# Kernel tuning notes

Hardware: AMD Instinct MI355X
Metric: run time of the kernel (lower is better)

Reference implementation:

```python
import jax, jax.numpy as jnp
import numpy as np

B, T, D = 8, 1024, 128
TEMP = 0.1
WEIGHT = 1.0


def _neg_scaled_l2(x, y):
    # x: [P, T, D], y: [P, S, D] -> -||x-y||^2 / D / TEMP  (l2 similarity, normalize_dimension=True)
    x2 = jnp.sum(x * x, axis=-1)[..., :, None]            # [P, T, 1]
    y2 = jnp.sum(y * y, axis=-1)[..., None, :]            # [P, 1, S]
    xy = jnp.einsum('ptd,psd->pts', x, y)                 # [P, T, S]
    d2 = jnp.maximum(x2 + y2 - 2.0 * xy, 0.0)             # cdist(...)**2 is non-negative
    return -d2 / D / TEMP


def setup_inputs() -> dict:
    key = jax.random.key(0)
    k1, k2, k3 = jax.random.split(key, 3)
    embs = jax.random.normal(k1, (B, T, D), dtype=jnp.float32)
    frame_idxs = jnp.sort(jax.random.randint(k2, (B, T), 0, 4096, dtype=jnp.int32), axis=-1)
    video_len = jax.random.randint(k3, (B,), T, 4096, dtype=jnp.int32)
    return {"embs": embs, "frame_idxs": frame_idxs, "video_len": video_len}


def reference(embs, frame_idxs, video_len):
    # All ordered pairs (i, j) with i != j, built at trace time.
    pairs = np.array([(i, j) for i in range(B) for j in range(B) if i != j])
    ii, jj = pairs[:, 0], pairs[:, 1]                     # [P]

    e1 = embs[ii]                                         # [P, T, D]
    e2 = embs[jj]                                         # [P, T, D]

    # Cycle: soft nearest neighbors of e1 in e2, then align back to e1.
    sim12 = _neg_scaled_l2(e1, e2)                        # [P, T, T]
    beta12 = jax.nn.softmax(sim12, axis=-1)
    nn_embs = jnp.einsum('pts,psd->ptd', beta12, e2)      # [P, T, D]
    logits = _neg_scaled_l2(nn_embs, e1)                  # [P, T, T]

    beta = jax.nn.softmax(logits, axis=-1)                # [P, T, T]
    steps = frame_idxs.astype(jnp.float32) / video_len.astype(jnp.float32)[:, None]  # [B, T]
    sp = steps[ii]                                        # [P, T] (steps of sequence i)
    time_true = sp                                        # one_hot(labels) picks the diagonal
    time_pred = jnp.einsum('pts,ps->pt', beta, sp)        # [P, T]
    loss = jnp.mean((time_pred - time_true) ** 2)
    return WEIGHT * loss
```

## Files before the change

### kernel.cpp

```cpp
#include <hip/hip_runtime.h>
#include <hip/hip_bf16.h>


#define T_ 1024
#define D_ 128
#define NPAIR 56
#define NSCALE 0.11271055006945026f
#define SQDS 0.474785316f

typedef float f32x16 __attribute__((ext_vector_type(16)));
typedef unsigned short u16x8 __attribute__((ext_vector_type(8)));

#define B8F 131072
#define B8T 163840

__device__ __forceinline__ unsigned short f2bf(float f) {
  unsigned u = __float_as_uint(f);
  u += 0x7fff + ((u >> 16) & 1);
  return (unsigned short)(u >> 16);
}
__device__ __forceinline__ float bf2f(unsigned short v) {
  return __uint_as_float(((unsigned)v) << 16);
}
__device__ __forceinline__ float clamp8(float x) {
  return fminf(fmaxf(x, -440.f), 440.f);
}
__device__ __forceinline__ unsigned pk4(float a, float b, float c, float d) {
  int w = __builtin_amdgcn_cvt_pk_fp8_f32(a, b, 0, false);
  w = __builtin_amdgcn_cvt_pk_fp8_f32(c, d, w, true);
  return (unsigned)w;
}
__device__ __forceinline__ float waveSum(float v) {
#pragma unroll
  for (int k = 32; k >= 1; k >>= 1) v += __shfl_xor(v, k, 64);
  return v;
}
__device__ __forceinline__ void stage1k(const unsigned char* g, unsigned char* lds, int lane) {
  __builtin_amdgcn_global_load_lds(
      (const __attribute__((address_space(1))) unsigned int*)(g + lane * 16),
      (__attribute__((address_space(3))) unsigned int*)lds, 16, 0, 0);
}

__device__ __forceinline__ void c2b8(const unsigned* m, int lh, long long* b0, long long* b1) {
  unsigned send0 = lh ? m[0] : m[1];
  unsigned send1 = lh ? m[2] : m[3];
  unsigned r0 = (unsigned)__shfl_xor((int)send0, 32, 64);
  unsigned r1 = (unsigned)__shfl_xor((int)send1, 32, 64);
  union { unsigned u[2]; long long ll; } x0, x1;
  x0.u[0] = lh ? r0 : m[0];  x0.u[1] = lh ? m[1] : r0;
  x1.u[0] = lh ? r1 : m[2];  x1.u[1] = lh ? m[3] : r1;
  *b0 = x0.ll; *b1 = x1.ll;
}

#define MFMA8(A, B, C) __builtin_amdgcn_mfma_f32_32x32x16_fp8_fp8((A), (B), (C), 0, 0, 0)
#define LD8(P, Q) (*(const long long*)((P) + (Q) * 512))
#define EXPC(x) fminf(__builtin_amdgcn_exp2f(x), 448.f)

__global__ __launch_bounds__(256) void convert_kernel(
    const float* __restrict__ embs, const int* __restrict__ fi,
    const int* __restrict__ vl, unsigned char* __restrict__ e8F,
    unsigned char* __restrict__ e8T, float* __restrict__ steps,
    float* __restrict__ acc, unsigned* __restrict__ cnt) {
  __shared__ unsigned short tileS[32 * 136];
  __shared__ float psum[32][8];
  __shared__ float g_sh[32], sp_sh[32];
  const int b = blockIdx.x >> 5;
  const int t0 = (blockIdx.x & 31) * 32;
  const int tid = threadIdx.x;
  const int row = tid >> 3, seg = tid & 7;

  if (blockIdx.x == 0 && tid == 0) { acc[0] = 0.f; cnt[0] = 0u; }

  const float* src = embs + (size_t)(b * T_ + t0 + row) * D_ + seg * 16;
  float4 g4[4];
#pragma unroll
  for (int k = 0; k < 4; k++) g4[k] = ((const float4*)src)[k];
  float s = 0.f;
  float fv[16];
#pragma unroll
  for (int k = 0; k < 4; k++) {
    s += g4[k].x * g4[k].x + g4[k].y * g4[k].y + g4[k].z * g4[k].z + g4[k].w * g4[k].w;
    fv[4 * k + 0] = g4[k].x * SQDS; fv[4 * k + 1] = g4[k].y * SQDS;
    fv[4 * k + 2] = g4[k].z * SQDS; fv[4 * k + 3] = g4[k].w * SQDS;
  }
  psum[row][seg] = s;

  {
    unsigned char* dstA = e8F + (size_t)b * B8F + (size_t)((t0 >> 5) * 8 + seg) * 512;
    uint2 lo, hi;
    lo.x = pk4(fv[0], fv[1], fv[2], fv[3]);   lo.y = pk4(fv[4], fv[5], fv[6], fv[7]);
    hi.x = pk4(fv[8], fv[9], fv[10], fv[11]); hi.y = pk4(fv[12], fv[13], fv[14], fv[15]);
    *(uint2*)(dstA + row * 8) = lo;
    *(uint2*)(dstA + (size_t)(32 + row) * 8) = hi;
  }
#pragma unroll
  for (int k = 0; k < 16; k++) tileS[row * 136 + seg * 16 + k] = f2bf(fv[k]);
  __syncthreads();

  if (tid < 32) {
    float t = 0.f;
#pragma unroll
    for (int k = 0; k < 8; k++) t += psum[tid][k];
    int gr = b * T_ + t0 + tid;
    float sp = (float)fi[gr] / (float)vl[b];
    steps[gr] = sp;
    sp_sh[tid] = sp;
    g_sh[tid] = __builtin_amdgcn_exp2f(14.0f - t * NSCALE);
  }
  __syncthreads();

  {
    const int c8 = tid >> 5;
    const int n2 = c8 & 3, scp = c8 >> 2;
    const int dd = n2 * 32 + (tid & 31);
#pragma unroll
    for (int half = 0; half < 2; half++) {
      const int lane = half * 32 + (tid & 31);
      const int sl = scp * 16 + half * 8;
      float vv[8];
#pragma unroll
      for (int jj = 0; jj < 8; jj++)
        vv[jj] = clamp8(bf2f(tileS[(sl + jj) * 136 + dd]) * g_sh[sl + jj]);
      uint2 wv;
      wv.x = pk4(vv[0], vv[1], vv[2], vv[3]);
      wv.y = pk4(vv[4], vv[5], vv[6], vv[7]);
      int c = n2 * 64 + (t0 >> 4) + scp;
      *(uint2*)(e8T + (size_t)b * B8T + (size_t)c * 512 + lane * 8) = wv;
    }
  }
  if (tid < 128) {
    const int sc2 = tid >> 6, lane = tid & 63;
    const int m = lane & 31, kh = lane >> 5;
    uint2 wv; wv.x = 0u; wv.y = 0u;
    if (m < 2) {
      float vv[8];
#pragma unroll
      for (int e = 0; e < 8; e++) {
        int sl = sc2 * 16 + kh * 8 + e;
        float gg = g_sh[sl];
        vv[e] = clamp8(m ? gg * sp_sh[sl] : gg);
      }
      wv.x = pk4(vv[0], vv[1], vv[2], vv[3]);
      wv.y = pk4(vv[4], vv[5], vv[6], vv[7]);
    }
    int c = 256 + (t0 >> 4) + sc2;
    *(uint2*)(e8T + (size_t)b * B8T + (size_t)c * 512 + lane * 8) = wv;
  }
}

__global__ __launch_bounds__(256, 2) void tcc_main(
    const unsigned char* __restrict__ e8F, const unsigned char* __restrict__ e8T,
    const float* __restrict__ steps, float* __restrict__ loss_acc,
    unsigned* __restrict__ cnt, float* __restrict__ out) {
  __shared__ unsigned char smem[40960];
  __shared__ float blred[4];
  unsigned char* kt = smem;
  unsigned char* vt = smem + 16384;
  unsigned char* gt = smem + 36864;

  const int bx = blockIdx.x;
  const int pair = bx >> 3;
  const int tile = bx & 7;
  const int i = pair / 7;
  const int r = pair % 7;
  const int j = r + (r >= i ? 1 : 0);
  const int tid = threadIdx.x;
  const int w = tid >> 6;
  const int l = tid & 63;
  const int l31 = l & 31;
  const int lh = l >> 5;
  const int tb = tile * 128 + w * 32;

  const unsigned char* eFi = e8F + (size_t)i * B8F;
  const unsigned char* eFj = e8F + (size_t)j * B8F;
  const unsigned char* eTj = e8T + (size_t)j * B8T;
  const unsigned char* eTi = e8T + (size_t)i * B8T;

  long long qf8[8];
  {
    const unsigned char* qb = eFi + (size_t)((tb >> 5) * 8) * 512 + l * 8;
#pragma unroll
    for (int kc = 0; kc < 8; kc++) qf8[kc] = LD8(qb, kc);
  }

  const f32x16 Z = {0.f, 0.f, 0.f, 0.f, 0.f, 0.f, 0.f, 0.f,
                    0.f, 0.f, 0.f, 0.f, 0.f, 0.f, 0.f, 0.f};
  const f32x16 CM6 = {-6.f, -6.f, -6.f, -6.f, -6.f, -6.f, -6.f, -6.f,
                      -6.f, -6.f, -6.f, -6.f, -6.f, -6.f, -6.f, -6.f};
  f32x16 o[5];
#pragma unroll
  for (int n2 = 0; n2 < 5; n2++) o[n2] = Z;

  stage1k(eFj + (size_t)(2 * w) * 1024, kt + (2 * w) * 1024, l);
  stage1k(eFj + (size_t)(2 * w + 1) * 1024, kt + (2 * w + 1) * 1024, l);
#pragma unroll
  for (int u = 0; u < 3; u++) {
    int vu = w + 4 * u;
    if (vu < 10) {
      int n2v = vu >> 1, sh = vu & 1;
      stage1k(eTj + (size_t)(n2v * 32 + sh) * 1024, vt + vu * 1024, l);
    }
  }
  __syncthreads();

  for (int st = 0; st < 16; st++) {
    const int cur = st & 1, nxt = cur ^ 1;
    if (st < 15) {
      const int s1 = st + 1;
      stage1k(eFj + (size_t)(8 * s1 + 2 * w) * 1024, kt + nxt * 8192 + (2 * w) * 1024, l);
      stage1k(eFj + (size_t)(8 * s1 + 2 * w + 1) * 1024, kt + nxt * 8192 + (2 * w + 1) * 1024, l);
#pragma unroll
      for (int u = 0; u < 3; u++) {
        int vu = w + 4 * u;
        if (vu < 10) {
          int n2v = vu >> 1, sh = vu & 1;
          stage1k(eTj + (size_t)(n2v * 32 + s1 * 2 + sh) * 1024, vt + nxt * 10240 + vu * 1024, l);
        }
      }
    }
    __builtin_amdgcn_sched_barrier(0);

    const unsigned char* kb = kt + cur * 8192 + l * 8;
    const unsigned char* vb = vt + cur * 10240 + l * 8;

    f32x16 ca0 = MFMA8(LD8(kb, 0), qf8[0], CM6);
    f32x16 ca1 = MFMA8(LD8(kb, 8), qf8[0], CM6);
#pragma unroll
    for (int dc = 1; dc < 8; dc++) {
      ca0 = MFMA8(LD8(kb, dc), qf8[dc], ca0);
      ca1 = MFMA8(LD8(kb, 8 + dc), qf8[dc], ca1);
    }
    unsigned m0[4], m1[4];
#pragma unroll
    for (int k2 = 0; k2 < 4; k2++) {
      m0[k2] = pk4(EXPC(ca0[4 * k2]), EXPC(ca0[4 * k2 + 1]),
                   EXPC(ca0[4 * k2 + 2]), EXPC(ca0[4 * k2 + 3]));
      m1[k2] = pk4(EXPC(ca1[4 * k2]), EXPC(ca1[4 * k2 + 1]),
                   EXPC(ca1[4 * k2 + 2]), EXPC(ca1[4 * k2 + 3]));
    }
    long long pB[4];
    c2b8(m0, lh, &pB[0], &pB[1]);
    c2b8(m1, lh, &pB[2], &pB[3]);
#pragma unroll
    for (int n2 = 0; n2 < 5; n2++)
#pragma unroll
      for (int sc = 0; sc < 4; sc++)
        o[n2] = MFMA8(LD8(vb, n2 * 4 + sc), pB[sc], o[n2]);
    __syncthreads();
  }

  stage1k(eFi + (size_t)(2 * w) * 1024, kt + (2 * w) * 1024, l);
  stage1k(eFi + (size_t)(2 * w + 1) * 1024, kt + (2 * w + 1) * 1024, l);
  if (w < 2) stage1k(eTi + (size_t)(128 + w) * 1024, gt + w * 1024, l);

  float Lme = o[4][0];
  float Lo = __shfl_xor(Lme, 32, 64);
  float inv = 1.0f / (lh ? Lo : Lme);
  long long qf2[8];
#pragma unroll
  for (int n2 = 0; n2 < 4; n2++) {
    unsigned mm[4];
#pragma unroll
    for (int k2 = 0; k2 < 4; k2++)
      mm[k2] = pk4(o[n2][4 * k2] * inv, o[n2][4 * k2 + 1] * inv,
                   o[n2][4 * k2 + 2] * inv, o[n2][4 * k2 + 3] * inv);
    c2b8(mm, lh, &qf2[2 * n2], &qf2[2 * n2 + 1]);
  }
  f32x16 acc6 = Z;
  __syncthreads();

  for (int st = 0; st < 16; st++) {
    const int cur = st & 1, nxt = cur ^ 1;
    if (st < 15) {
      const int s1 = st + 1;
      stage1k(eFi + (size_t)(8 * s1 + 2 * w) * 1024, kt + nxt * 8192 + (2 * w) * 1024, l);
      stage1k(eFi + (size_t)(8 * s1 + 2 * w + 1) * 1024, kt + nxt * 8192 + (2 * w + 1) * 1024, l);
      if (w < 2) stage1k(eTi + (size_t)(128 + s1 * 2 + w) * 1024, gt + nxt * 2048 + w * 1024, l);
    }
    __builtin_amdgcn_sched_barrier(0);

    const unsigned char* kb = kt + cur * 8192 + l * 8;
    const unsigned char* gb = gt + cur * 2048 + l * 8;

    f32x16 ca0 = MFMA8(LD8(kb, 0), qf2[0], CM6);
    f32x16 ca1 = MFMA8(LD8(kb, 8), qf2[0], CM6);
#pragma unroll
    for (int dc = 1; dc < 8; dc++) {
      ca0 = MFMA8(LD8(kb, dc), qf2[dc], ca0);
      ca1 = MFMA8(LD8(kb, 8 + dc), qf2[dc], ca1);
    }
    unsigned m0[4], m1[4];
#pragma unroll
    for (int k2 = 0; k2 < 4; k2++) {
      m0[k2] = pk4(EXPC(ca0[4 * k2]), EXPC(ca0[4 * k2 + 1]),
                   EXPC(ca0[4 * k2 + 2]), EXPC(ca0[4 * k2 + 3]));
      m1[k2] = pk4(EXPC(ca1[4 * k2]), EXPC(ca1[4 * k2 + 1]),
                   EXPC(ca1[4 * k2 + 2]), EXPC(ca1[4 * k2 + 3]));
    }
    long long pB[4];
    c2b8(m0, lh, &pB[0], &pB[1]);
    c2b8(m1, lh, &pB[2], &pB[3]);
#pragma unroll
    for (int sc = 0; sc < 4; sc++)
      acc6 = MFMA8(LD8(gb, sc), pB[sc], acc6);
    __syncthreads();
  }

  float local = 0.f;
  if (lh == 0) {
    float pred = acc6[1] / acc6[0];
    float tt = steps[i * T_ + tb + l31];
    float dd = pred - tt;
    local = dd * dd;
  }
  local = waveSum(local);
  if (l == 0) blred[w] = local;
  __syncthreads();
  if (tid == 0) {
    atomicAdd(loss_acc, blred[0] + blred[1] + blred[2] + blred[3]);
    __threadfence();
    unsigned old = atomicAdd(cnt, 1u);
    if (old == (unsigned)(gridDim.x - 1)) {
      float v = atomicAdd(loss_acc, 0.0f);
      out[0] = v * (1.0f / (float)(NPAIR * T_));
    }
  }
}

extern "C" void kernel_launch(void* const* d_in, const int* in_sizes, int n_in,
                              void* d_out, int out_size, void* d_ws, size_t ws_size,
                              hipStream_t stream) {
  const float* embs = (const float*)d_in[0];
  const int* frame_idxs = (const int*)d_in[1];
  const int* video_len = (const int*)d_in[2];
  float* out = (float*)d_out;

  char* ws = (char*)d_ws;
  float* acc = (float*)ws;
  unsigned* cnt = (unsigned*)(ws + 512);
  float* steps = (float*)(ws + 4096);
  unsigned char* e8F = (unsigned char*)(ws + 65536);
  unsigned char* e8T = e8F + (size_t)8 * B8F;

  convert_kernel<<<dim3(256), dim3(256), 0, stream>>>(embs, frame_idxs, video_len,
                                                      e8F, e8T, steps, acc, cnt);
  tcc_main<<<dim3(NPAIR * 8), dim3(256), 0, stream>>>(e8F, e8T, steps, acc, cnt, out);
}
```

Before: 114.5 us.

## Split key dimension across warp pairs and double grid with cross-warp reduction

Each block now covers 64 query rows instead of 128. The four warps split into two row groups, each handling half of every 32-key stage (split-K). Partial flash-attention accumulators are combined through shared memory, and the normalized second-stage queries are shared the same way. The grid doubles to 896 blocks and launch bounds ask for 3 blocks per CU to improve occupancy and CU fill. In exchange, global staging traffic per row doubles and extra LDS reductions and barriers are added.

```diff
diff --git a/kernel.cpp b/kernel.cpp
--- a/kernel.cpp
+++ b/kernel.cpp
@@ -148,28 +148,30 @@
   }
 }
 
-__global__ __launch_bounds__(256, 2) void tcc_main(
+__global__ __launch_bounds__(256, 3) void tcc_main(
     const unsigned char* __restrict__ e8F, const unsigned char* __restrict__ e8T,
     const float* __restrict__ steps, float* __restrict__ loss_acc,
     unsigned* __restrict__ cnt, float* __restrict__ out) {
-  __shared__ unsigned char smem[40960];
+  __shared__ unsigned char smem[49152];
   __shared__ float blred[4];
   unsigned char* kt = smem;
   unsigned char* vt = smem + 16384;
   unsigned char* gt = smem + 36864;
 
   const int bx = blockIdx.x;
-  const int pair = bx >> 3;
-  const int tile = bx & 7;
+  const int pair = bx >> 4;
+  const int tile = bx & 15;
   const int i = pair / 7;
   const int r = pair % 7;
   const int j = r + (r >= i ? 1 : 0);
   const int tid = threadIdx.x;
   const int w = tid >> 6;
+  const int rg = w & 1;
+  const int sh = w >> 1;
   const int l = tid & 63;
   const int l31 = l & 31;
   const int lh = l >> 5;
-  const int tb = tile * 128 + w * 32;
+  const int tb = tile * 64 + rg * 32;
 
   const unsigned char* eFi = e8F + (size_t)i * B8F;
   const unsigned char* eFj = e8F + (size_t)j * B8F;
@@ -197,8 +199,8 @@
   for (int u = 0; u < 3; u++) {
     int vu = w + 4 * u;
     if (vu < 10) {
-      int n2v = vu >> 1, sh = vu & 1;
-      stage1k(eTj + (size_t)(n2v * 32 + sh) * 1024, vt + vu * 1024, l);
+      int n2v = vu >> 1, uh = vu & 1;
+      stage1k(eTj + (size_t)(n2v * 32 + uh) * 1024, vt + vu * 1024, l);
     }
   }
   __syncthreads();
@@ -213,59 +215,76 @@
       for (int u = 0; u < 3; u++) {
         int vu = w + 4 * u;
         if (vu < 10) {
-          int n2v = vu >> 1, sh = vu & 1;
-          stage1k(eTj + (size_t)(n2v * 32 + s1 * 2 + sh) * 1024, vt + nxt * 10240 + vu * 1024, l);
+          int n2v = vu >> 1, uh = vu & 1;
+          stage1k(eTj + (size_t)(n2v * 32 + s1 * 2 + uh) * 1024, vt + nxt * 10240 + vu * 1024, l);
         }
       }
     }
     __builtin_amdgcn_sched_barrier(0);
 
-    const unsigned char* kb = kt + cur * 8192 + l * 8;
-    const unsigned char* vb = vt + cur * 10240 + l * 8;
-
-    f32x16 ca0 = MFMA8(LD8(kb, 0), qf8[0], CM6);
-    f32x16 ca1 = MFMA8(LD8(kb, 8), qf8[0], CM6);
-#pragma unroll
-    for (int dc = 1; dc < 8; dc++) {
-      ca0 = MFMA8(LD8(kb, dc), qf8[dc], ca0);
-      ca1 = MFMA8(LD8(kb, 8 + dc), qf8[dc], ca1);
-    }
-    unsigned m0[4], m1[4];
-#pragma unroll
-    for (int k2 = 0; k2 < 4; k2++) {
-      m0[k2] = pk4(EXPC(ca0[4 * k2]), EXPC(ca0[4 * k2 + 1]),
-                   EXPC(ca0[4 * k2 + 2]), EXPC(ca0[4 * k2 + 3]));
-      m1[k2] = pk4(EXPC(ca1[4 * k2]), EXPC(ca1[4 * k2 + 1]),
-                   EXPC(ca1[4 * k2 + 2]), EXPC(ca1[4 * k2 + 3]));
-    }
-    long long pB[4];
+    const unsigned char* kb = kt + cur * 8192 + sh * 4096 + l * 8;
+    const unsigned char* vb = vt + cur * 10240 + sh * 1024 + l * 8;
+
+    f32x16 ca = MFMA8(LD8(kb, 0), qf8[0], CM6);
+#pragma unroll
+    for (int dc = 1; dc < 8; dc++) ca = MFMA8(LD8(kb, dc), qf8[dc], ca);
+    unsigned m0[4];
+#pragma unroll
+    for (int k2 = 0; k2 < 4; k2++)
+      m0[k2] = pk4(EXPC(ca[4 * k2]), EXPC(ca[4 * k2 + 1]),
+                   EXPC(ca[4 * k2 + 2]), EXPC(ca[4 * k2 + 3]));
+    long long pB[2];
     c2b8(m0, lh, &pB[0], &pB[1]);
-    c2b8(m1, lh, &pB[2], &pB[3]);
 #pragma unroll
     for (int n2 = 0; n2 < 5; n2++)
 #pragma unroll
-      for (int sc = 0; sc < 4; sc++)
+      for (int sc = 0; sc < 2; sc++)
         o[n2] = MFMA8(LD8(vb, n2 * 4 + sc), pB[sc], o[n2]);
     __syncthreads();
+  }
+
+  float* xb = (float*)smem;
+  if (sh == 1) {
+#pragma unroll
+    for (int n2 = 0; n2 < 5; n2++)
+#pragma unroll
+      for (int rr = 0; rr < 16; rr++)
+        xb[(n2 * 16 + rr) * 128 + rg * 64 + l] = o[n2][rr];
+  }
+  __syncthreads();
+  long long qf2[8];
+  if (sh == 0) {
+#pragma unroll
+    for (int n2 = 0; n2 < 5; n2++)
+#pragma unroll
+      for (int rr = 0; rr < 16; rr++)
+        o[n2][rr] += xb[(n2 * 16 + rr) * 128 + rg * 64 + l];
+    float Lme = o[4][0];
+    float Lo = __shfl_xor(Lme, 32, 64);
+    float inv = 1.0f / (lh ? Lo : Lme);
+#pragma unroll
+    for (int n2 = 0; n2 < 4; n2++) {
+      unsigned mm[4];
+#pragma unroll
+      for (int k2 = 0; k2 < 4; k2++)
+        mm[k2] = pk4(o[n2][4 * k2] * inv, o[n2][4 * k2 + 1] * inv,
+                     o[n2][4 * k2 + 2] * inv, o[n2][4 * k2 + 3] * inv);
+      c2b8(mm, lh, &qf2[2 * n2], &qf2[2 * n2 + 1]);
+    }
+    long long* qb2 = (long long*)(smem + 40960);
+#pragma unroll
+    for (int kc = 0; kc < 8; kc++) qb2[kc * 128 + rg * 64 + l] = qf2[kc];
+  }
+  __syncthreads();
+  if (sh == 1) {
+    const long long* qb2 = (const long long*)(smem + 40960);
+#pragma unroll
+    for (int kc = 0; kc < 8; kc++) qf2[kc] = qb2[kc * 128 + rg * 64 + l];
   }
 
   stage1k(eFi + (size_t)(2 * w) * 1024, kt + (2 * w) * 1024, l);
   stage1k(eFi + (size_t)(2 * w + 1) * 1024, kt + (2 * w + 1) * 1024, l);
   if (w < 2) stage1k(eTi + (size_t)(128 + w) * 1024, gt + w * 1024, l);
-
-  float Lme = o[4][0];
-  float Lo = __shfl_xor(Lme, 32, 64);
-  float inv = 1.0f / (lh ? Lo : Lme);
-  long long qf2[8];
-#pragma unroll
-  for (int n2 = 0; n2 < 4; n2++) {
-    unsigned mm[4];
-#pragma unroll
-    for (int k2 = 0; k2 < 4; k2++)
-      mm[k2] = pk4(o[n2][4 * k2] * inv, o[n2][4 * k2 + 1] * inv,
-                   o[n2][4 * k2 + 2] * inv, o[n2][4 * k2 + 3] * inv);
-    c2b8(mm, lh, &qf2[2 * n2], &qf2[2 * n2 + 1]);
-  }
   f32x16 acc6 = Z;
   __syncthreads();
 
@@ -279,36 +298,36 @@
     }
     __builtin_amdgcn_sched_barrier(0);
 
-    const unsigned char* kb = kt + cur * 8192 + l * 8;
-    const unsigned char* gb = gt + cur * 2048 + l * 8;
-
-    f32x16 ca0 = MFMA8(LD8(kb, 0), qf2[0], CM6);
-    f32x16 ca1 = MFMA8(LD8(kb, 8), qf2[0], CM6);
-#pragma unroll
-    for (int dc = 1; dc < 8; dc++) {
-      ca0 = MFMA8(LD8(kb, dc), qf2[dc], ca0);
-      ca1 = MFMA8(LD8(kb, 8 + dc), qf2[dc], ca1);
-    }
-    unsigned m0[4], m1[4];
-#pragma unroll
-    for (int k2 = 0; k2 < 4; k2++) {
-      m0[k2] = pk4(EXPC(ca0[4 * k2]), EXPC(ca0[4 * k2 + 1]),
-                   EXPC(ca0[4 * k2 + 2]), EXPC(ca0[4 * k2 + 3]));
-      m1[k2] = pk4(EXPC(ca1[4 * k2]), EXPC(ca1[4 * k2 + 1]),
-                   EXPC(ca1[4 * k2 + 2]), EXPC(ca1[4 * k2 + 3]));
-    }
-    long long pB[4];
+    const unsigned char* kb = kt + cur * 8192 + sh * 4096 + l * 8;
+    const unsigned char* gb = gt + cur * 2048 + sh * 1024 + l * 8;
+
+    f32x16 ca = MFMA8(LD8(kb, 0), qf2[0], CM6);
+#pragma unroll
+    for (int dc = 1; dc < 8; dc++) ca = MFMA8(LD8(kb, dc), qf2[dc], ca);
+    unsigned m0[4];
+#pragma unroll
+    for (int k2 = 0; k2 < 4; k2++)
+      m0[k2] = pk4(EXPC(ca[4 * k2]), EXPC(ca[4 * k2 + 1]),
+                   EXPC(ca[4 * k2 + 2]), EXPC(ca[4 * k2 + 3]));
+    long long pB[2];
     c2b8(m0, lh, &pB[0], &pB[1]);
-    c2b8(m1, lh, &pB[2], &pB[3]);
-#pragma unroll
-    for (int sc = 0; sc < 4; sc++)
+#pragma unroll
+    for (int sc = 0; sc < 2; sc++)
       acc6 = MFMA8(LD8(gb, sc), pB[sc], acc6);
     __syncthreads();
   }
 
+  float* ab = (float*)(smem + 40960);
+  if (sh == 1) {
+    ab[(rg * 64 + l) * 2] = acc6[0];
+    ab[(rg * 64 + l) * 2 + 1] = acc6[1];
+  }
+  __syncthreads();
   float local = 0.f;
-  if (lh == 0) {
-    float pred = acc6[1] / acc6[0];
+  if (sh == 0 && lh == 0) {
+    float L2v = acc6[0] + ab[(rg * 64 + l) * 2];
+    float tpv = acc6[1] + ab[(rg * 64 + l) * 2 + 1];
+    float pred = tpv / L2v;
     float tt = steps[i * T_ + tb + l31];
     float dd = pred - tt;
     local = dd * dd;
@@ -344,5 +363,5 @@
 
   convert_kernel<<<dim3(256), dim3(256), 0, stream>>>(embs, frame_idxs, video_len,
                                                       e8F, e8T, steps, acc, cnt);
-  tcc_main<<<dim3(NPAIR * 8), dim3(256), 0, stream>>>(e8F, e8T, steps, acc, cnt, out);
-}
+  tcc_main<<<dim3(NPAIR * 16), dim3(256), 0, stream>>>(e8F, e8T, steps, acc, cnt, out);
+}
```

After: 130.9 us. 1.14x slower.

## Triple-buffer LDS staging with partial vmcnt waits and raw barriers

Applied to the files above, without the earlier changes.

Replaces the double-buffered LDS pipeline in both attention phases with a three-stage ring buffer that prefetches two steps ahead. A partial s_waitcnt vmcnt, tuned per wave to its number of outstanding async loads, lets each wave wait only for the oldest stage before a raw s_barrier, instead of a full __syncthreads drain. The goal is to hide global-to-LDS latency better. In exchange LDS use grows to about 54 KB per block, which may limit occupancy at two blocks per CU, and correctness now rests on hand-counted vmcnt values.

```diff
diff --git a/kernel.cpp b/kernel.cpp
--- a/kernel.cpp
+++ b/kernel.cpp
@@ -55,6 +55,8 @@
 #define MFMA8(A, B, C) __builtin_amdgcn_mfma_f32_32x32x16_fp8_fp8((A), (B), (C), 0, 0, 0)
 #define LD8(P, Q) (*(const long long*)((P) + (Q) * 512))
 #define EXPC(x) fminf(__builtin_amdgcn_exp2f(x), 448.f)
+#define WAITV(N) asm volatile("s_waitcnt vmcnt(" #N ")" ::: "memory")
+#define BAR() do { asm volatile("" ::: "memory"); __builtin_amdgcn_s_barrier(); asm volatile("" ::: "memory"); } while (0)
 
 __global__ __launch_bounds__(256) void convert_kernel(
     const float* __restrict__ embs, const int* __restrict__ fi,
@@ -152,11 +154,11 @@
     const unsigned char* __restrict__ e8F, const unsigned char* __restrict__ e8T,
     const float* __restrict__ steps, float* __restrict__ loss_acc,
     unsigned* __restrict__ cnt, float* __restrict__ out) {
-  __shared__ unsigned char smem[40960];
+  __shared__ unsigned char smem[55296];
   __shared__ float blred[4];
   unsigned char* kt = smem;
-  unsigned char* vt = smem + 16384;
-  unsigned char* gt = smem + 36864;
+  unsigned char* vt = smem + 24576;
+  unsigned char* gt = smem + 24576;
 
   const int bx = blockIdx.x;
   const int pair = bx >> 3;
@@ -191,67 +193,78 @@
 #pragma unroll
   for (int n2 = 0; n2 < 5; n2++) o[n2] = Z;
 
-  stage1k(eFj + (size_t)(2 * w) * 1024, kt + (2 * w) * 1024, l);
-  stage1k(eFj + (size_t)(2 * w + 1) * 1024, kt + (2 * w + 1) * 1024, l);
-#pragma unroll
-  for (int u = 0; u < 3; u++) {
-    int vu = w + 4 * u;
-    if (vu < 10) {
-      int n2v = vu >> 1, sh = vu & 1;
-      stage1k(eTj + (size_t)(n2v * 32 + sh) * 1024, vt + vu * 1024, l);
-    }
-  }
-  __syncthreads();
-
-  for (int st = 0; st < 16; st++) {
-    const int cur = st & 1, nxt = cur ^ 1;
-    if (st < 15) {
-      const int s1 = st + 1;
-      stage1k(eFj + (size_t)(8 * s1 + 2 * w) * 1024, kt + nxt * 8192 + (2 * w) * 1024, l);
-      stage1k(eFj + (size_t)(8 * s1 + 2 * w + 1) * 1024, kt + nxt * 8192 + (2 * w + 1) * 1024, l);
-#pragma unroll
-      for (int u = 0; u < 3; u++) {
-        int vu = w + 4 * u;
-        if (vu < 10) {
-          int n2v = vu >> 1, sh = vu & 1;
-          stage1k(eTj + (size_t)(n2v * 32 + s1 * 2 + sh) * 1024, vt + nxt * 10240 + vu * 1024, l);
-        }
-      }
-    }
-    __builtin_amdgcn_sched_barrier(0);
-
-    const unsigned char* kb = kt + cur * 8192 + l * 8;
-    const unsigned char* vb = vt + cur * 10240 + l * 8;
-
-    f32x16 ca0 = MFMA8(LD8(kb, 0), qf8[0], CM6);
-    f32x16 ca1 = MFMA8(LD8(kb, 8), qf8[0], CM6);
-#pragma unroll
-    for (int dc = 1; dc < 8; dc++) {
-      ca0 = MFMA8(LD8(kb, dc), qf8[dc], ca0);
-      ca1 = MFMA8(LD8(kb, 8 + dc), qf8[dc], ca1);
-    }
-    unsigned m0[4], m1[4];
-#pragma unroll
-    for (int k2 = 0; k2 < 4; k2++) {
-      m0[k2] = pk4(EXPC(ca0[4 * k2]), EXPC(ca0[4 * k2 + 1]),
-                   EXPC(ca0[4 * k2 + 2]), EXPC(ca0[4 * k2 + 3]));
-      m1[k2] = pk4(EXPC(ca1[4 * k2]), EXPC(ca1[4 * k2 + 1]),
-                   EXPC(ca1[4 * k2 + 2]), EXPC(ca1[4 * k2 + 3]));
-    }
-    long long pB[4];
-    c2b8(m0, lh, &pB[0], &pB[1]);
-    c2b8(m1, lh, &pB[2], &pB[3]);
-#pragma unroll
-    for (int n2 = 0; n2 < 5; n2++)
-#pragma unroll
-      for (int sc = 0; sc < 4; sc++)
-        o[n2] = MFMA8(LD8(vb, n2 * 4 + sc), pB[sc], o[n2]);
-    __syncthreads();
-  }
-
-  stage1k(eFi + (size_t)(2 * w) * 1024, kt + (2 * w) * 1024, l);
-  stage1k(eFi + (size_t)(2 * w + 1) * 1024, kt + (2 * w + 1) * 1024, l);
-  if (w < 2) stage1k(eTi + (size_t)(128 + w) * 1024, gt + w * 1024, l);
+  auto stageP1 = [&](int t, int b) {
+    stage1k(eFj + (size_t)(8 * t + 2 * w) * 1024, kt + b * 8192 + (2 * w) * 1024, l);
+    stage1k(eFj + (size_t)(8 * t + 2 * w + 1) * 1024, kt + b * 8192 + (2 * w + 1) * 1024, l);
+#pragma unroll
+    for (int u = 0; u < 3; u++) {
+      int vu = w + 4 * u;
+      if (vu < 10) {
+        int n2v = vu >> 1, uh = vu & 1;
+        stage1k(eTj + (size_t)(n2v * 32 + t * 2 + uh) * 1024, vt + b * 10240 + vu * 1024, l);
+      }
+    }
+  };
+  auto stageP2 = [&](int t, int b) {
+    stage1k(eFi + (size_t)(8 * t + 2 * w) * 1024, kt + b * 8192 + (2 * w) * 1024, l);
+    stage1k(eFi + (size_t)(8 * t + 2 * w + 1) * 1024, kt + b * 8192 + (2 * w + 1) * 1024, l);
+    if (w < 2) stage1k(eTi + (size_t)(128 + t * 2 + w) * 1024, gt + b * 2048 + w * 1024, l);
+  };
+
+  stageP1(0, 0);
+  stageP1(1, 1);
+  if (w < 2) WAITV(5); else WAITV(4);
+  BAR();
+
+  {
+    int cur = 0, pre = 2;
+    for (int st = 0; st < 16; st++) {
+      if (st <= 13) stageP1(st + 2, pre);
+      __builtin_amdgcn_sched_barrier(0);
+
+      const unsigned char* kb = kt + cur * 8192 + l * 8;
+      const unsigned char* vb = vt + cur * 10240 + l * 8;
+
+      f32x16 ca0 = MFMA8(LD8(kb, 0), qf8[0], CM6);
+      f32x16 ca1 = MFMA8(LD8(kb, 8), qf8[0], CM6);
+#pragma unroll
+      for (int dc = 1; dc < 8; dc++) {
+        ca0 = MFMA8(LD8(kb, dc), qf8[dc], ca0);
+        ca1 = MFMA8(LD8(kb, 8 + dc), qf8[dc], ca1);
+      }
+      unsigned m0[4], m1[4];
+#pragma unroll
+      for (int k2 = 0; k2 < 4; k2++) {
+        m0[k2] = pk4(EXPC(ca0[4 * k2]), EXPC(ca0[4 * k2 + 1]),
+                     EXPC(ca0[4 * k2 + 2]), EXPC(ca0[4 * k2 + 3]));
+        m1[k2] = pk4(EXPC(ca1[4 * k2]), EXPC(ca1[4 * k2 + 1]),
+                     EXPC(ca1[4 * k2 + 2]), EXPC(ca1[4 * k2 + 3]));
+      }
+      long long pB[4];
+      c2b8(m0, lh, &pB[0], &pB[1]);
+      c2b8(m1, lh, &pB[2], &pB[3]);
+#pragma unroll
+      for (int n2 = 0; n2 < 5; n2++)
+#pragma unroll
+        for (int sc = 0; sc < 4; sc++)
+          o[n2] = MFMA8(LD8(vb, n2 * 4 + sc), pB[sc], o[n2]);
+
+      if (st <= 13) {
+        if (w < 2) WAITV(5); else WAITV(4);
+        BAR();
+      } else if (st == 14) {
+        WAITV(0);
+        BAR();
+      } else {
+        BAR();
+      }
+      cur = (cur == 2) ? 0 : cur + 1;
+      pre = (pre == 2) ? 0 : pre + 1;
+    }
+  }
+
+  stageP2(0, 0);
+  stageP2(1, 1);
 
   float Lme = o[4][0];
   float Lo = __shfl_xor(Lme, 32, 64);
@@ -267,43 +280,50 @@
     c2b8(mm, lh, &qf2[2 * n2], &qf2[2 * n2 + 1]);
   }
   f32x16 acc6 = Z;
-  __syncthreads();
-
-  for (int st = 0; st < 16; st++) {
-    const int cur = st & 1, nxt = cur ^ 1;
-    if (st < 15) {
-      const int s1 = st + 1;
-      stage1k(eFi + (size_t)(8 * s1 + 2 * w) * 1024, kt + nxt * 8192 + (2 * w) * 1024, l);
-      stage1k(eFi + (size_t)(8 * s1 + 2 * w + 1) * 1024, kt + nxt * 8192 + (2 * w + 1) * 1024, l);
-      if (w < 2) stage1k(eTi + (size_t)(128 + s1 * 2 + w) * 1024, gt + nxt * 2048 + w * 1024, l);
-    }
-    __builtin_amdgcn_sched_barrier(0);
-
-    const unsigned char* kb = kt + cur * 8192 + l * 8;
-    const unsigned char* gb = gt + cur * 2048 + l * 8;
-
-    f32x16 ca0 = MFMA8(LD8(kb, 0), qf2[0], CM6);
-    f32x16 ca1 = MFMA8(LD8(kb, 8), qf2[0], CM6);
-#pragma unroll
-    for (int dc = 1; dc < 8; dc++) {
-      ca0 = MFMA8(LD8(kb, dc), qf2[dc], ca0);
-      ca1 = MFMA8(LD8(kb, 8 + dc), qf2[dc], ca1);
-    }
-    unsigned m0[4], m1[4];
-#pragma unroll
-    for (int k2 = 0; k2 < 4; k2++) {
-      m0[k2] = pk4(EXPC(ca0[4 * k2]), EXPC(ca0[4 * k2 + 1]),
-                   EXPC(ca0[4 * k2 + 2]), EXPC(ca0[4 * k2 + 3]));
-      m1[k2] = pk4(EXPC(ca1[4 * k2]), EXPC(ca1[4 * k2 + 1]),
-                   EXPC(ca1[4 * k2 + 2]), EXPC(ca1[4 * k2 + 3]));
-    }
-    long long pB[4];
-    c2b8(m0, lh, &pB[0], &pB[1]);
-    c2b8(m1, lh, &pB[2], &pB[3]);
-#pragma unroll
-    for (int sc = 0; sc < 4; sc++)
-      acc6 = MFMA8(LD8(gb, sc), pB[sc], acc6);
-    __syncthreads();
+  if (w < 2) WAITV(3); else WAITV(2);
+  BAR();
+
+  {
+    int cur = 0, pre = 2;
+    for (int st = 0; st < 16; st++) {
+      if (st <= 13) stageP2(st + 2, pre);
+      __builtin_amdgcn_sched_barrier(0);
+
+      const unsigned char* kb = kt + cur * 8192 + l * 8;
+      const unsigned char* gb = gt + cur * 2048 + l * 8;
+
+      f32x16 ca0 = MFMA8(LD8(kb, 0), qf2[0], CM6);
+      f32x16 ca1 = MFMA8(LD8(kb, 8), qf2[0], CM6);
+#pragma unroll
+      for (int dc = 1; dc < 8; dc++) {
+        ca0 = MFMA8(LD8(kb, dc), qf2[dc], ca0);
+        ca1 = MFMA8(LD8(kb, 8 + dc), qf2[dc], ca1);
+      }
+      unsigned m0[4], m1[4];
+#pragma unroll
+      for (int k2 = 0; k2 < 4; k2++) {
+        m0[k2] = pk4(EXPC(ca0[4 * k2]), EXPC(ca0[4 * k2 + 1]),
+                     EXPC(ca0[4 * k2 + 2]), EXPC(ca0[4 * k2 + 3]));
+        m1[k2] = pk4(EXPC(ca1[4 * k2]), EXPC(ca1[4 * k2 + 1]),
+                     EXPC(ca1[4 * k2 + 2]), EXPC(ca1[4 * k2 + 3]));
+      }
+      long long pB[4];
+      c2b8(m0, lh, &pB[0], &pB[1]);
+      c2b8(m1, lh, &pB[2], &pB[3]);
+#pragma unroll
+      for (int sc = 0; sc < 4; sc++)
+        acc6 = MFMA8(LD8(gb, sc), pB[sc], acc6);
+
+      if (st <= 13) {
+        if (w < 2) WAITV(3); else WAITV(2);
+        BAR();
+      } else if (st == 14) {
+        WAITV(0);
+        BAR();
+      }
+      cur = (cur == 2) ? 0 : cur + 1;
+      pre = (pre == 2) ? 0 : pre + 1;
+    }
   }
 
   float local = 0.f;
```

Measured after the change: 117.5 us. +2.6%, slower.

## Read K/V fp8 operands directly from global memory instead of LDS staging

Applied to the files above, without the earlier changes.

Removes the double-buffered global_load_lds staging of key, value and step tiles into shared memory along with the per-iteration block barriers. Each wave now loads its MFMA operands straight from global memory (relying on L1/L2 caching), which cuts LDS usage and synchronisation. The cost is that every wave fetches the same tiles redundantly, with no software prefetch to overlap load latency with MFMA work.

```diff
diff --git a/kernel.cpp b/kernel.cpp
--- a/kernel.cpp
+++ b/kernel.cpp
@@ -9,7 +9,6 @@
 #define SQDS 0.474785316f
 
 typedef float f32x16 __attribute__((ext_vector_type(16)));
-typedef unsigned short u16x8 __attribute__((ext_vector_type(8)));
 
 #define B8F 131072
 #define B8T 163840
@@ -34,11 +33,6 @@
 #pragma unroll
   for (int k = 32; k >= 1; k >>= 1) v += __shfl_xor(v, k, 64);
   return v;
-}
-__device__ __forceinline__ void stage1k(const unsigned char* g, unsigned char* lds, int lane) {
-  __builtin_amdgcn_global_load_lds(
-      (const __attribute__((address_space(1))) unsigned int*)(g + lane * 16),
-      (__attribute__((address_space(3))) unsigned int*)lds, 16, 0, 0);
 }
 
 __device__ __forceinline__ void c2b8(const unsigned* m, int lh, long long* b0, long long* b1) {
@@ -152,11 +146,7 @@
     const unsigned char* __restrict__ e8F, const unsigned char* __restrict__ e8T,
     const float* __restrict__ steps, float* __restrict__ loss_acc,
     unsigned* __restrict__ cnt, float* __restrict__ out) {
-  __shared__ unsigned char smem[40960];
   __shared__ float blred[4];
-  unsigned char* kt = smem;
-  unsigned char* vt = smem + 16384;
-  unsigned char* gt = smem + 36864;
 
   const int bx = blockIdx.x;
   const int pair = bx >> 3;
@@ -191,37 +181,9 @@
 #pragma unroll
   for (int n2 = 0; n2 < 5; n2++) o[n2] = Z;
 
-  stage1k(eFj + (size_t)(2 * w) * 1024, kt + (2 * w) * 1024, l);
-  stage1k(eFj + (size_t)(2 * w + 1) * 1024, kt + (2 * w + 1) * 1024, l);
-#pragma unroll
-  for (int u = 0; u < 3; u++) {
-    int vu = w + 4 * u;
-    if (vu < 10) {
-      int n2v = vu >> 1, sh = vu & 1;
-      stage1k(eTj + (size_t)(n2v * 32 + sh) * 1024, vt + vu * 1024, l);
-    }
-  }
-  __syncthreads();
-
   for (int st = 0; st < 16; st++) {
-    const int cur = st & 1, nxt = cur ^ 1;
-    if (st < 15) {
-      const int s1 = st + 1;
-      stage1k(eFj + (size_t)(8 * s1 + 2 * w) * 1024, kt + nxt * 8192 + (2 * w) * 1024, l);
-      stage1k(eFj + (size_t)(8 * s1 + 2 * w + 1) * 1024, kt + nxt * 8192 + (2 * w + 1) * 1024, l);
-#pragma unroll
-      for (int u = 0; u < 3; u++) {
-        int vu = w + 4 * u;
-        if (vu < 10) {
-          int n2v = vu >> 1, sh = vu & 1;
-          stage1k(eTj + (size_t)(n2v * 32 + s1 * 2 + sh) * 1024, vt + nxt * 10240 + vu * 1024, l);
-        }
-      }
-    }
-    __builtin_amdgcn_sched_barrier(0);
-
-    const unsigned char* kb = kt + cur * 8192 + l * 8;
-    const unsigned char* vb = vt + cur * 10240 + l * 8;
+    const unsigned char* kb = eFj + (size_t)(st * 16) * 512 + l * 8;
+    const unsigned char* vb = eTj + (size_t)(st * 4) * 512 + l * 8;
 
     f32x16 ca0 = MFMA8(LD8(kb, 0), qf8[0], CM6);
     f32x16 ca1 = MFMA8(LD8(kb, 8), qf8[0], CM6);
@@ -245,13 +207,8 @@
     for (int n2 = 0; n2 < 5; n2++)
 #pragma unroll
       for (int sc = 0; sc < 4; sc++)
-        o[n2] = MFMA8(LD8(vb, n2 * 4 + sc), pB[sc], o[n2]);
-    __syncthreads();
-  }
-
-  stage1k(eFi + (size_t)(2 * w) * 1024, kt + (2 * w) * 1024, l);
-  stage1k(eFi + (size_t)(2 * w + 1) * 1024, kt + (2 * w + 1) * 1024, l);
-  if (w < 2) stage1k(eTi + (size_t)(128 + w) * 1024, gt + w * 1024, l);
+        o[n2] = MFMA8(LD8(vb, n2 * 64 + sc), pB[sc], o[n2]);
+  }
 
   float Lme = o[4][0];
   float Lo = __shfl_xor(Lme, 32, 64);
@@ -267,20 +224,10 @@
     c2b8(mm, lh, &qf2[2 * n2], &qf2[2 * n2 + 1]);
   }
   f32x16 acc6 = Z;
-  __syncthreads();
 
   for (int st = 0; st < 16; st++) {
-    const int cur = st & 1, nxt = cur ^ 1;
-    if (st < 15) {
-      const int s1 = st + 1;
-      stage1k(eFi + (size_t)(8 * s1 + 2 * w) * 1024, kt + nxt * 8192 + (2 * w) * 1024, l);
-      stage1k(eFi + (size_t)(8 * s1 + 2 * w + 1) * 1024, kt + nxt * 8192 + (2 * w + 1) * 1024, l);
-      if (w < 2) stage1k(eTi + (size_t)(128 + s1 * 2 + w) * 1024, gt + nxt * 2048 + w * 1024, l);
-    }
-    __builtin_amdgcn_sched_barrier(0);
-
-    const unsigned char* kb = kt + cur * 8192 + l * 8;
-    const unsigned char* gb = gt + cur * 2048 + l * 8;
+    const unsigned char* kb = eFi + (size_t)(st * 16) * 512 + l * 8;
+    const unsigned char* gb = eTi + (size_t)(256 + st * 4) * 512 + l * 8;
 
     f32x16 ca0 = MFMA8(LD8(kb, 0), qf2[0], CM6);
     f32x16 ca1 = MFMA8(LD8(kb, 8), qf2[0], CM6);
@@ -303,7 +250,6 @@
 #pragma unroll
     for (int sc = 0; sc < 4; sc++)
       acc6 = MFMA8(LD8(gb, sc), pB[sc], acc6);
-    __syncthreads();
   }
 
   float local = 0.f;
```

Result: slower. 133.7 us (+16.8%).
